# Kernel optimization log

Measured on AMD Instinct MI355X. Metric: run time of the kernel, lower is better.

Reference implementation:

```python
import jax, jax.numpy as jnp
import numpy as np

N, E, G = 5000, 10000, 200
EPS = 1e-5


def _nnconv(x, edge_attr, src, dst, w1, b1, w2, b2, root, bias, din, dout):
    # edge MLP -> per-edge weight matrix [E, din, dout]
    h = jax.nn.relu(edge_attr @ w1 + b1)
    We = (h @ w2 + b2).reshape(-1, din, dout)
    # gather source node feats, per-edge bmm, scatter-mean to targets
    msg = jnp.einsum('ei,eio->eo', x[src], We)  # [E, dout]
    s = jax.ops.segment_sum(msg, dst, num_segments=N)
    cnt = jax.ops.segment_sum(jnp.ones((msg.shape[0],), msg.dtype), dst, num_segments=N)
    agg = s / jnp.maximum(cnt, 1.0)[:, None]
    return agg + x @ root + bias


def _bn(x, g, b, m, v):
    return (x - m) * (g / jnp.sqrt(v + EPS)) + b


def setup_inputs() -> dict:
    key = jax.random.key(0)
    ks = iter(jax.random.split(key, 64))
    d = {}
    d['x'] = jax.random.normal(next(ks), (N, 15), jnp.float32)
    d['edge_attr'] = jax.random.normal(next(ks), (E, 3), jnp.float32)
    d['edge_index'] = jax.random.randint(next(ks), (2, E), 0, N, jnp.int32)
    d['batch'] = jnp.sort(jax.random.randint(next(ks), (N,), 0, G, jnp.int32))
    d['atom_num'] = jnp.zeros((G,), jnp.int32)
    dims = [(15, 64), (64, 128), (128, 256)]
    for l, (din, dout) in enumerate(dims, start=1):
        d[f'nn{l}_w1'] = jax.random.normal(next(ks), (3, 32), jnp.float32) * 0.1
        d[f'nn{l}_b1'] = jnp.zeros((32,), jnp.float32)
        d[f'nn{l}_w2'] = jax.random.normal(next(ks), (32, din * dout), jnp.float32) * 0.05
        d[f'nn{l}_b2'] = jnp.zeros((din * dout,), jnp.float32)
        d[f'root{l}'] = jax.random.normal(next(ks), (din, dout), jnp.float32) * 0.1
        d[f'bias{l}'] = jnp.zeros((dout,), jnp.float32)
        d[f'bn{l}_g'] = jnp.ones((dout,), jnp.float32)
        d[f'bn{l}_b'] = jnp.zeros((dout,), jnp.float32)
        d[f'bn{l}_m'] = jnp.zeros((dout,), jnp.float32)
        d[f'bn{l}_v'] = jnp.ones((dout,), jnp.float32)
    d['mlp_w'] = jax.random.normal(next(ks), (256, 200), jnp.float32) * 0.05
    d['mlp_b'] = jnp.zeros((200,), jnp.float32)
    return d


def reference(x, edge_attr, edge_index, batch, atom_num,
              nn1_w1, nn1_b1, nn1_w2, nn1_b2, root1, bias1, bn1_g, bn1_b, bn1_m, bn1_v,
              nn2_w1, nn2_b1, nn2_w2, nn2_b2, root2, bias2, bn2_g, bn2_b, bn2_m, bn2_v,
              nn3_w1, nn3_b1, nn3_w2, nn3_b2, root3, bias3, bn3_g, bn3_b, bn3_m, bn3_v,
              mlp_w, mlp_b):
    src, dst = edge_index[0], edge_index[1]
    h = _nnconv(x, edge_attr, src, dst, nn1_w1, nn1_b1, nn1_w2, nn1_b2, root1, bias1, 15, 64)
    h = jax.nn.relu(_bn(h, bn1_g, bn1_b, bn1_m, bn1_v))
    h = _nnconv(h, edge_attr, src, dst, nn2_w1, nn2_b1, nn2_w2, nn2_b2, root2, bias2, 64, 128)
    h = jax.nn.relu(_bn(h, bn2_g, bn2_b, bn2_m, bn2_v))
    h = _nnconv(h, edge_attr, src, dst, nn3_w1, nn3_b1, nn3_w2, nn3_b2, root3, bias3, 128, 256)
    h = jax.nn.relu(_bn(h, bn3_g, bn3_b, bn3_m, bn3_v))
    node_rep = h
    # per-graph node counts, exclusive cumulative offsets
    ones = jnp.ones((N,), h.dtype)
    counts = jax.ops.segment_sum(ones, batch, num_segments=G)  # [G]
    offsets = (jnp.cumsum(counts) - counts).astype(jnp.int32)
    idx = atom_num + offsets
    node_embedding = node_rep[idx]  # [G, 256]
    # global mean pool
    gsum = jax.ops.segment_sum(h, batch, num_segments=G)
    graph_embedding = gsum / jnp.maximum(counts, 1.0)[:, None]
    h_new = 0.5 * graph_embedding + node_embedding
    out = h_new @ mlp_w + mlp_b
    return out, node_embedding
```

## Files before the change

### kernel.cpp

```cpp
#include <hip/hip_runtime.h>
#include <stdint.h>

#define DEVINL __device__ __forceinline__

typedef __attribute__((ext_vector_type(8))) __bf16 bf16x8;
typedef __attribute__((ext_vector_type(8))) short s16x8;
typedef __attribute__((ext_vector_type(4))) float f32x4;

constexpr int NN = 5000;
constexpr int NE = 10000;
constexpr int NG = 200;
constexpr int BM = 64;
constexpr int MBLK = (NE + BM - 1) / BM;
constexpr int EROWS = MBLK * BM;
constexpr int SBLK = (NN + BM - 1) / BM;
constexpr int SROWS = SBLK * BM;
constexpr int NKP = 36;
constexpr int PHKT = 4;
constexpr int NBUF = 3;

DEVINL short f2bf(float f) {
  union { float f; unsigned u; } v; v.f = f;
  unsigned u = v.u + 0x7fffu + ((v.u >> 16) & 1u);
  return (short)(u >> 16);
}

DEVINL void gload16(const void* g, void* l) {
  __builtin_amdgcn_global_load_lds(
      (const __attribute__((address_space(1))) void*)g,
      (__attribute__((address_space(3))) void*)l, 16, 0, 0);
}


template <int DIN_DATA, int DIN_PAD, int DOUT>
DEVINL void buildB_one(int idx, const float* w2, const float* b2,
                       const float* root, short* Bp) {
  int cc = idx & 3;
  int n = (idx >> 2) % DOUT;
  int kt = (idx >> 2) / DOUT;
  int kap0 = kt * 32 + cc * 8;
  s16x8 v;
#pragma unroll
  for (int j = 0; j < 8; ++j) {
    int kap = kap0 + j;
    int k = kap / DIN_PAD, i = kap % DIN_PAD;
    float val = 0.f;
    if (i < DIN_DATA && k <= 33)
      val = (k < 32) ? w2[(size_t)(k * DIN_DATA + i) * DOUT + n]
                     : (k == 32) ? b2[(size_t)i * DOUT + n]
                                 : root[(size_t)i * DOUT + n];
    v[j] = f2bf(val);
  }
  int swz = cc ^ ((n >> 1) & 3);
  *(s16x8*)((char*)Bp + (size_t)kt * DOUT * 64 + n * 64 + swz * 16) = v;
}

constexpr int BCH1 = (NKP * 32 / 8) * 64;
constexpr int BCH2 = (NKP * 64 / 8) * 128;
constexpr int BCH3 = (NKP * 128 / 8) * 256;
constexpr int EMB = (EROWS + 255) / 256;
constexpr int PREPB = (NN * 32 + 255) / 256;
constexpr int BLDB = (BCH1 + BCH2 + BCH3 + 255) / 256;


__global__ void setup(const float* ea, const int* dst, const int* batch,
                      const float* x0,
                      const float* w1a, const float* b1a,
                      const float* w1b, const float* b1b,
                      const float* w1c, const float* b1c,
                      const float* w2a, const float* b2a, const float* ra,
                      const float* w2b, const float* b2b, const float* rb,
                      const float* w2c, const float* b2c, const float* rc,
                      short* hta, short* htb, short* htc,
                      short* Bp1, short* Bp2, short* Bp3,
                      float* cnt, float* gcnt, short* xbf0) {
  int b = blockIdx.x, t = threadIdx.x;
  if (b < 3 * EMB) {
    int L = b / EMB, eb = b % EMB;
    const float* w1 = (L == 0) ? w1a : (L == 1) ? w1b : w1c;
    const float* b1 = (L == 0) ? b1a : (L == 1) ? b1b : b1c;
    short* ht = (L == 0) ? hta : (L == 1) ? htb : htc;
    int e = eb * 256 + t;
    if (e >= EROWS) return;
    bool ve = e < NE;
    float a0 = 0, a1 = 0, a2 = 0;
    if (ve) { a0 = ea[e * 3]; a1 = ea[e * 3 + 1]; a2 = ea[e * 3 + 2]; }
    for (int k = 0; k < NKP; ++k) {
      float v = 0.f;
      if (ve) {
        if (k < 32) {
          float x = b1[k] + a0 * w1[k] + a1 * w1[32 + k] + a2 * w1[64 + k];
          v = x > 0.f ? x : 0.f;
        } else if (k == 32) {
          v = 1.0f;
        }
      }
      ht[(size_t)k * EROWS + e] = f2bf(v);
    }
  } else if (b < 3 * EMB + PREPB) {
    int idx = (b - 3 * EMB) * 256 + t;
    if (idx < NE) atomicAdd(&cnt[dst[idx]], 1.0f);
    if (idx < NN) atomicAdd(&gcnt[batch[idx]], 1.0f);
    if (idx < NN * 32) {
      int n = idx >> 5, i = idx & 31;
      xbf0[idx] = (i < 15) ? f2bf(x0[n * 15 + i]) : (short)0;
    }
  } else {
    int idx = (b - 3 * EMB - PREPB) * 256 + t;
    if (idx < BCH1) {
      buildB_one<15, 32, 64>(idx, w2a, b2a, ra, Bp1);
    } else if (idx < BCH1 + BCH2) {
      buildB_one<64, 64, 128>(idx - BCH1, w2b, b2b, rb, Bp2);
    } else if (idx < BCH1 + BCH2 + BCH3) {
      buildB_one<128, 128, 256>(idx - BCH1 - BCH2, w2c, b2c, rc, Bp3);
    }
  }
}


__global__ void node_scan(const float* cnt, int* noff, int* fill) {
  constexpr int PT = (NN + 1023) / 1024;
  __shared__ int s[1024];
  int t = threadIdx.x;
  int loc[PT];
  int sum = 0;
#pragma unroll
  for (int q = 0; q < PT; ++q) {
    int i = t * PT + q;
    loc[q] = sum;
    sum += (i < NN) ? (int)cnt[i] : 0;
  }
  s[t] = sum;
  __syncthreads();
  for (int d = 1; d < 1024; d <<= 1) {
    int u = (t >= d) ? s[t - d] : 0;
    __syncthreads();
    s[t] += u;
    __syncthreads();
  }
  int base = s[t] - sum;
#pragma unroll
  for (int q = 0; q < PT; ++q) {
    int i = t * PT + q;
    if (i < NN) { noff[i] = base + loc[q]; fill[i] = 0; }
  }
}

__global__ void csr_fill(const int* dst, const int* noff, int* fill, int* elist) {
  int e = blockIdx.x * 256 + threadIdx.x;
  if (e < NE) {
    int n = dst[e];
    int p = noff[n] + atomicAdd(&fill[n], 1);
    elist[p] = e;
  }
}


template <int DIN_PAD, int DOUT, int NSPLIT, int NKPE>
__launch_bounds__(512)
__global__ void fused_gemm(const short* xbf, const short* ht, const short* Bp,
                           const int* srcI, float* Pout) {
  constexpr int NI = DIN_PAD / 32;
  constexpr int ROWB = DIN_PAD * 2;
  constexpr int CHPR = ROWB / 16;
  constexpr int CHLOG = (CHPR == 4) ? 2 : (CHPR == 8) ? 3 : 4;
  constexpr int SWZM = (CHPR >= 8) ? 7 : 3;
  constexpr int DOUT_L = DOUT / NSPLIT;
  constexpr int MT = 2;
  constexpr int KT_TOTAL = NKPE * NI;
  constexpr int NPH = KT_TOTAL / PHKT;
  static_assert(KT_TOTAL % PHKT == 0, "phase align");
  static_assert(PHKT % NI == 0 || NI % PHKT == 0, "k align");
  constexpr int PHB = PHKT * DOUT_L * 64;
  constexpr int CPK = DOUT_L * 4;
  constexpr int CH = PHKT * CPK;
  constexpr int XGB = BM * ROWB;
  constexpr int SMB = (XGB > NBUF * PHB) ? XGB : NBUF * PHB;

  __shared__ __align__(16) char smem[SMB];
  __shared__ __align__(16) short hs[NKPE * BM];
  __shared__ int src_s[BM];

  const int t = threadIdx.x, lane = t & 63, w = t >> 6;
  const int wm = w >> 2, wn = w & 3;
  const bool isSelf = (blockIdx.x >= MBLK);
  const int m0 = (isSelf ? (blockIdx.x - MBLK) : blockIdx.x) * BM;
  const int bn0 = blockIdx.y * DOUT_L;
  if (t < BM) {
    int r = m0 + t;
    src_s[t] = isSelf ? ((r < NN) ? r : 0) : ((r < NE) ? srcI[r] : 0);
  }
  __syncthreads();

  constexpr int XCH = BM * CHPR;
#pragma unroll
  for (int rd = 0; rd < (XCH + 511) / 512; ++rd) {
    int L = rd * 512 + t;
    if (XCH % 512 == 0 || L < XCH) {
      int r = L >> CHLOG, pch = L & (CHPR - 1);
      int j = pch ^ (r & SWZM);
      gload16((const char*)xbf + (size_t)src_s[r] * ROWB + j * 16,
              (char*)smem + (size_t)L * 16);
    }
  }
  if (!isSelf && t < NKPE * (BM / 8)) {
    int kl = t >> 3, c = t & 7;
    gload16((const char*)ht + ((size_t)kl * EROWS + m0) * 2 + c * 16,
            (char*)hs + (size_t)t * 16);
  }
  __syncthreads();

  bf16x8 afr[NI][MT];
#pragma unroll
  for (int ii = 0; ii < NI; ++ii)
#pragma unroll
    for (int mt = 0; mt < MT; ++mt) {
      int r = wm * 32 + mt * 16 + (lane & 15);
      int c = ii * 4 + (lane >> 4);
      int pos = c ^ (r & SWZM);
      afr[ii][mt] = *(const bf16x8*)((const char*)smem + r * ROWB + pos * 16);
    }
  asm volatile("s_waitcnt lgkmcnt(0)" ::: "memory");
  __builtin_amdgcn_sched_barrier(0);
  __builtin_amdgcn_s_barrier();

  const char* Bg = (const char*)Bp + (size_t)bn0 * 64;

  f32x4 msg[MT], part[MT];
#pragma unroll
  for (int mt = 0; mt < MT; ++mt)
#pragma unroll
    for (int i = 0; i < 4; ++i) { msg[mt][i] = 0.f; part[mt][i] = 0.f; }

  if (isSelf) {
    constexpr int KT0 = 33 * NI;
    constexpr int CHS = NI * CPK;
#pragma unroll
    for (int cc = 0; cc < (CHS + 511) / 512; ++cc) {
      int idx = cc * 512 + t;
      if (CHS % 512 == 0 || idx < CHS) {
        int ktl = idx / CPK, win = idx % CPK;
        gload16(Bg + (size_t)(KT0 + ktl) * (DOUT * 64) + (size_t)win * 16,
                (char*)smem + (size_t)idx * 16);
      }
    }
    asm volatile("s_waitcnt vmcnt(0)" ::: "memory");
    __builtin_amdgcn_s_barrier();
    __builtin_amdgcn_sched_barrier(0);
#pragma unroll
    for (int j = 0; j < NI; ++j) {
      bf16x8 bfr;
      {
        int n = wn * 16 + (lane & 15);
        int cch = (lane >> 4) ^ ((n >> 1) & 3);
        bfr = *(const bf16x8*)((const char*)smem + j * (DOUT_L * 64) + n * 64 +
                               cch * 16);
      }
#pragma unroll
      for (int mt = 0; mt < MT; ++mt)
        msg[mt] = __builtin_amdgcn_mfma_f32_16x16x32_bf16(afr[j][mt], bfr,
                                                          msg[mt], 0, 0, 0);
    }
    float* P = Pout + (size_t)(EROWS + m0) * DOUT + bn0;
#pragma unroll
    for (int mt = 0; mt < MT; ++mt) {
      int col = wn * 16 + (lane & 15);
#pragma unroll
      for (int reg = 0; reg < 4; ++reg) {
        int r = wm * 32 + mt * 16 + (lane >> 4) * 4 + reg;
        P[(size_t)r * DOUT + col] = msg[mt][reg];
      }
    }
    return;
  }

  auto stageB = [&](int ph, int buf) {
    char* dstB = (char*)smem + buf * PHB;
#pragma unroll
    for (int cc = 0; cc < CH / 512; ++cc) {
      int idx = cc * 512 + t;
      int ktl = idx / CPK;
      int win = idx % CPK;
      gload16(Bg + (size_t)(ph * PHKT + ktl) * (DOUT * 64) + (size_t)win * 16,
              dstB + (size_t)idx * 16);
    }
  };

  stageB(0, 0);
  if (NPH > 1) stageB(1, 1);
  if (NPH > 2) stageB(2, 2);
  for (int ph = 0; ph < NPH; ++ph) {
    if (ph + 2 < NPH) {
      asm volatile("s_waitcnt vmcnt(4)" ::: "memory");
    } else if (ph + 1 < NPH) {
      asm volatile("s_waitcnt vmcnt(2)" ::: "memory");
    } else {
      asm volatile("s_waitcnt vmcnt(0)" ::: "memory");
    }
    __builtin_amdgcn_s_barrier();
    __builtin_amdgcn_sched_barrier(0);
    const char* buf = (const char*)smem + (ph % NBUF) * PHB;
#pragma unroll
    for (int j = 0; j < PHKT; ++j) {
      const int kt = ph * PHKT + j;
      bf16x8 bfr;
      {
        int n = wn * 16 + (lane & 15);
        int cch = (lane >> 4) ^ ((n >> 1) & 3);
        bfr = *(const bf16x8*)(buf + j * (DOUT_L * 64) + n * 64 + cch * 16);
      }
#pragma unroll
      for (int mt = 0; mt < MT; ++mt)
        part[mt] = __builtin_amdgcn_mfma_f32_16x16x32_bf16(
            afr[j % NI][mt], bfr, part[mt], 0, 0, 0);
      if ((j % NI) == NI - 1) {
        int kl = kt / NI;
#pragma unroll
        for (int mt = 0; mt < MT; ++mt) {
          int rb = wm * 32 + mt * 16 + (lane >> 4) * 4;
          ushort4 hv = *(const ushort4*)((const char*)hs + (size_t)(kl * BM + rb) * 2);
          float h0, h1, h2, h3;
          { union { unsigned u; float f; } c;
            c.u = (unsigned)hv.x << 16; h0 = c.f;
            c.u = (unsigned)hv.y << 16; h1 = c.f;
            c.u = (unsigned)hv.z << 16; h2 = c.f;
            c.u = (unsigned)hv.w << 16; h3 = c.f; }
          msg[mt][0] += h0 * part[mt][0];
          msg[mt][1] += h1 * part[mt][1];
          msg[mt][2] += h2 * part[mt][2];
          msg[mt][3] += h3 * part[mt][3];
#pragma unroll
          for (int i = 0; i < 4; ++i) part[mt][i] = 0.f;
        }
      }
    }
    __builtin_amdgcn_sched_barrier(0);
    __builtin_amdgcn_s_barrier();
    if (ph + NBUF < NPH) stageB(ph + NBUF, (ph + NBUF) % NBUF);
  }
  float* P = Pout + (size_t)m0 * DOUT + bn0;
#pragma unroll
  for (int mt = 0; mt < MT; ++mt) {
    int col = wn * 16 + (lane & 15);
#pragma unroll
    for (int reg = 0; reg < 4; ++reg) {
      int r = wm * 32 + mt * 16 + (lane >> 4) * 4 + reg;
      P[(size_t)r * DOUT + col] = msg[mt][reg];
    }
  }
}


template <int DOUT>
__launch_bounds__(256)
__global__ void post_node(const float* P, const float* cnt, const int* noff,
                          const int* elist, const float* bias, const float* bg,
                          const float* bb, const float* bm, const float* bv,
                          float* xout, short* xbf) {
  constexpr int NPB = 8;
  constexpr int OS = 256 / DOUT;
  constexpr int NPT = NPB / OS;
  __shared__ int offs[NPB], cnts[NPB];
  int n0 = blockIdx.x * NPB;
  int t = threadIdx.x;
  int o = t % DOUT;
  int ng = t / DOUT;
  if (t < NPB) {
    int n = n0 + t;
    offs[t] = (n < NN) ? noff[n] : 0;
    cnts[t] = (n < NN) ? (int)cnt[n] : 0;
  }
  __syncthreads();
  float bi = bias[o];
  float scale = bg[o] * rsqrtf(bv[o] + 1e-5f);
  float mo = bm[o], bo = bb[o];
#pragma unroll
  for (int q = 0; q < NPT; ++q) {
    int nn = ng + q * OS;
    int n = n0 + nn;
    if (n >= NN) continue;
    int off = offs[nn], c = cnts[nn];
    float s = 0.f;
    for (int j = 0; j < c; ++j) {
      int e = elist[off + j];
      s += P[(size_t)e * DOUT + o];
    }
    float selfv = P[(size_t)(EROWS + n) * DOUT + o];
    float accv = s / fmaxf((float)c, 1.f) + selfv + bi;
    float v = (accv - mo) * scale + bo;
    v = v > 0.f ? v : 0.f;
    if (xout) xout[(size_t)n * DOUT + o] = v;
    if (xbf) xbf[(size_t)n * DOUT + o] = f2bf(v);
  }
}


__global__ void finish(const float* gcnt, const int* atom, const float* x3,
                       const float* mw, const float* mb, float* out) {
  __shared__ float red[256];
  __shared__ float hnew[256];
  int g = blockIdx.x, t = threadIdx.x;
  red[t] = (t < NG && t < g) ? gcnt[t] : 0.f;
  __syncthreads();
#pragma unroll
  for (int d = 128; d > 0; d >>= 1) {
    if (t < d) red[t] += red[t + d];
    __syncthreads();
  }
  int st = (int)red[0];
  int cn = (int)gcnt[g];
  int id = st + atom[g];
  id = id < 0 ? 0 : (id > NN - 1 ? NN - 1 : id);
  float s = 0.f;
  for (int n = st; n < st + cn; ++n) s += x3[(size_t)n * 256 + t];
  float ge = s / fmaxf((float)cn, 1.f);
  float ne = x3[(size_t)id * 256 + t];
  out[40000 + g * 256 + t] = ne;
  hnew[t] = 0.5f * ge + ne;
  __syncthreads();
  if (t < 200) {
    float a = mb[t];
#pragma unroll 8
    for (int oo = 0; oo < 256; ++oo) a += hnew[oo] * mw[(size_t)oo * 200 + t];
    out[g * 200 + t] = a;
  }
}


template <int DIN_PAD, int DOUT, int NSPLIT, int NKPE>
static void run_layer(void* const* d_in, int l, const int* srcI,
                      const short* xbf_in, float* xout_f32, short* xbf_out,
                      float* Pbuf, const float* cnt, const int* noff,
                      const int* elist, const short* ht, const short* Bp,
                      hipStream_t stream) {
  int base = 5 + (l - 1) * 10;
  const float* bias = (const float*)d_in[base + 5];
  const float* bg = (const float*)d_in[base + 6];
  const float* bb = (const float*)d_in[base + 7];
  const float* bm = (const float*)d_in[base + 8];
  const float* bv = (const float*)d_in[base + 9];

  fused_gemm<DIN_PAD, DOUT, NSPLIT, NKPE>
      <<<dim3(MBLK + SBLK, NSPLIT), 512, 0, stream>>>(xbf_in, ht, Bp, srcI, Pbuf);
  post_node<DOUT><<<(NN + 7) / 8, 256, 0, stream>>>(
      Pbuf, cnt, noff, elist, bias, bg, bb, bm, bv, xout_f32, xbf_out);
}

extern "C" void kernel_launch(void* const* d_in, const int* in_sizes, int n_in,
                              void* d_out, int out_size, void* d_ws, size_t ws_size,
                              hipStream_t stream) {
  (void)in_sizes; (void)n_in; (void)out_size; (void)ws_size;
  const float* x0 = (const float*)d_in[0];
  const float* ea = (const float*)d_in[1];
  const int* eidx = (const int*)d_in[2];
  const int* batch = (const int*)d_in[3];
  const int* atom = (const int*)d_in[4];
  const float* mw = (const float*)d_in[35];
  const float* mb = (const float*)d_in[36];
  const int* srcI = eidx;
  const int* dstI = eidx + NE;
  float* out = (float*)d_out;

  char* p = (char*)d_ws;
  auto alloc = [&](size_t bytes) {
    char* r = p;
    p += (bytes + 255) & ~size_t(255);
    return r;
  };
  float* xA = (float*)alloc((size_t)NN * 256 * 4);
  float* Pbuf = (float*)alloc((size_t)(EROWS + SROWS) * 256 * 4);
  float* cnt = (float*)alloc(NN * 4);
  int* noff = (int*)alloc(NN * 4);
  int* fill = (int*)alloc(NN * 4);
  int* elist = (int*)alloc(NE * 4);
  float* gcnt = (float*)alloc(NG * 4);
  short* ht1 = (short*)alloc((size_t)NKP * EROWS * 2);
  short* ht2 = (short*)alloc((size_t)NKP * EROWS * 2);
  short* ht3 = (short*)alloc((size_t)NKP * EROWS * 2);
  short* Bp1 = (short*)alloc((size_t)NKP * 32 * 64 * 2);
  short* Bp2 = (short*)alloc((size_t)NKP * 64 * 128 * 2);
  short* Bp3 = (short*)alloc((size_t)NKP * 128 * 256 * 2);
  short* xbf0 = (short*)alloc((size_t)NN * 32 * 2);
  short* xbfA = (short*)alloc((size_t)NN * 64 * 2);
  short* xbfB = (short*)alloc((size_t)NN * 128 * 2);

  hipMemsetAsync(cnt, 0, NN * 4, stream);
  hipMemsetAsync(gcnt, 0, NG * 4, stream);
  setup<<<3 * EMB + PREPB + BLDB, 256, 0, stream>>>(
      ea, dstI, batch, x0,
      (const float*)d_in[5], (const float*)d_in[6],
      (const float*)d_in[15], (const float*)d_in[16],
      (const float*)d_in[25], (const float*)d_in[26],
      (const float*)d_in[7], (const float*)d_in[8], (const float*)d_in[9],
      (const float*)d_in[17], (const float*)d_in[18], (const float*)d_in[19],
      (const float*)d_in[27], (const float*)d_in[28], (const float*)d_in[29],
      ht1, ht2, ht3, Bp1, Bp2, Bp3, cnt, gcnt, xbf0);
  node_scan<<<1, 1024, 0, stream>>>(cnt, noff, fill);
  csr_fill<<<(NE + 255) / 256, 256, 0, stream>>>(dstI, noff, fill, elist);

  run_layer<32, 64, 1, 36>(d_in, 1, srcI, xbf0, (float*)nullptr, xbfA, Pbuf,
                           cnt, noff, elist, ht1, Bp1, stream);
  run_layer<64, 128, 2, 34>(d_in, 2, srcI, xbfA, (float*)nullptr, xbfB, Pbuf,
                            cnt, noff, elist, ht2, Bp2, stream);
  run_layer<128, 256, 4, 33>(d_in, 3, srcI, xbfB, xA, (short*)nullptr, Pbuf,
                             cnt, noff, elist, ht3, Bp3, stream);

  finish<<<NG, 256, 0, stream>>>(gcnt, atom, xA, mw, mb, out);
}
```

Baseline: 260.9 us.

## Fold CSR build into setup, use fp32 edge hidden, larger layer-3 tile

Moves the node count, prefix scan, CSR fill and graph-count work into one extra block of the setup kernel using shared-memory atomics. This removes two memsets and the separate node_scan and csr_fill launches. The edge-MLP hidden values are now stored in fp32 instead of bf16, which drops the unpack step in the GEMM at the cost of twice the hidden-value traffic and LDS. The GEMM takes its row tile as a template parameter and layer 3 uses 128-row tiles. post_node now derives counts from consecutive offsets and stages the edge list in shared memory when it fits.

New measurement: 258.7 us. Within noise of the previous version (-0.8%).

```diff
diff --git a/kernel.cpp b/kernel.cpp
--- a/kernel.cpp
+++ b/kernel.cpp
@@ -10,11 +10,8 @@
 constexpr int NN = 5000;
 constexpr int NE = 10000;
 constexpr int NG = 200;
-constexpr int BM = 64;
-constexpr int MBLK = (NE + BM - 1) / BM;
-constexpr int EROWS = MBLK * BM;
-constexpr int SBLK = (NN + BM - 1) / BM;
-constexpr int SROWS = SBLK * BM;
+constexpr int EROWS = 10112;
+constexpr int SROWSMX = 5120;
 constexpr int NKP = 36;
 constexpr int PHKT = 4;
 constexpr int NBUF = 3;
@@ -58,29 +55,29 @@
 constexpr int BCH1 = (NKP * 32 / 8) * 64;
 constexpr int BCH2 = (NKP * 64 / 8) * 128;
 constexpr int BCH3 = (NKP * 128 / 8) * 256;
-constexpr int EMB = (EROWS + 255) / 256;
-constexpr int PREPB = (NN * 32 + 255) / 256;
-constexpr int BLDB = (BCH1 + BCH2 + BCH3 + 255) / 256;
-
-
-__global__ void setup(const float* ea, const int* dst, const int* batch,
-                      const float* x0,
-                      const float* w1a, const float* b1a,
-                      const float* w1b, const float* b1b,
-                      const float* w1c, const float* b1c,
-                      const float* w2a, const float* b2a, const float* ra,
-                      const float* w2b, const float* b2b, const float* rb,
-                      const float* w2c, const float* b2c, const float* rc,
-                      short* hta, short* htb, short* htc,
-                      short* Bp1, short* Bp2, short* Bp3,
-                      float* cnt, float* gcnt, short* xbf0) {
+constexpr int EMB = (EROWS + 1023) / 1024;
+constexpr int CASTB = (NN * 32 + 1023) / 1024;
+constexpr int BLDB = (BCH1 + BCH2 + BCH3 + 1023) / 1024;
+constexpr int SETUPB = 3 * EMB + CASTB + BLDB + 1;
+
+
+__global__ __launch_bounds__(1024) void setup(
+    const float* ea, const int* dst, const int* batch, const float* x0,
+    const float* w1a, const float* b1a, const float* w1b, const float* b1b,
+    const float* w1c, const float* b1c,
+    const float* w2a, const float* b2a, const float* ra,
+    const float* w2b, const float* b2b, const float* rb,
+    const float* w2c, const float* b2c, const float* rc,
+    float* hta, float* htb, float* htc,
+    short* Bp1, short* Bp2, short* Bp3,
+    short* xbf0, int* noff, int* elist, float* gcnt) {
   int b = blockIdx.x, t = threadIdx.x;
   if (b < 3 * EMB) {
     int L = b / EMB, eb = b % EMB;
     const float* w1 = (L == 0) ? w1a : (L == 1) ? w1b : w1c;
     const float* b1 = (L == 0) ? b1a : (L == 1) ? b1b : b1c;
-    short* ht = (L == 0) ? hta : (L == 1) ? htb : htc;
-    int e = eb * 256 + t;
+    float* ht = (L == 0) ? hta : (L == 1) ? htb : htc;
+    int e = eb * 1024 + t;
     if (e >= EROWS) return;
     bool ve = e < NE;
     float a0 = 0, a1 = 0, a2 = 0;
@@ -95,18 +92,16 @@
           v = 1.0f;
         }
       }
-      ht[(size_t)k * EROWS + e] = f2bf(v);
-    }
-  } else if (b < 3 * EMB + PREPB) {
-    int idx = (b - 3 * EMB) * 256 + t;
-    if (idx < NE) atomicAdd(&cnt[dst[idx]], 1.0f);
-    if (idx < NN) atomicAdd(&gcnt[batch[idx]], 1.0f);
+      ht[(size_t)k * EROWS + e] = v;
+    }
+  } else if (b < 3 * EMB + CASTB) {
+    int idx = (b - 3 * EMB) * 1024 + t;
     if (idx < NN * 32) {
       int n = idx >> 5, i = idx & 31;
       xbf0[idx] = (i < 15) ? f2bf(x0[n * 15 + i]) : (short)0;
     }
-  } else {
-    int idx = (b - 3 * EMB - PREPB) * 256 + t;
+  } else if (b < 3 * EMB + CASTB + BLDB) {
+    int idx = (b - 3 * EMB - CASTB) * 1024 + t;
     if (idx < BCH1) {
       buildB_one<15, 32, 64>(idx, w2a, b2a, ra, Bp1);
     } else if (idx < BCH1 + BCH2) {
@@ -114,59 +109,68 @@
     } else if (idx < BCH1 + BCH2 + BCH3) {
       buildB_one<128, 128, 256>(idx - BCH1 - BCH2, w2c, b2c, rc, Bp3);
     }
-  }
-}
-
-
-__global__ void node_scan(const float* cnt, int* noff, int* fill) {
-  constexpr int PT = (NN + 1023) / 1024;
-  __shared__ int s[1024];
-  int t = threadIdx.x;
-  int loc[PT];
-  int sum = 0;
-#pragma unroll
-  for (int q = 0; q < PT; ++q) {
-    int i = t * PT + q;
-    loc[q] = sum;
-    sum += (i < NN) ? (int)cnt[i] : 0;
-  }
-  s[t] = sum;
-  __syncthreads();
-  for (int d = 1; d < 1024; d <<= 1) {
-    int u = (t >= d) ? s[t - d] : 0;
+  } else {
+    __shared__ int cntL[NN];
+    __shared__ int sS[1024];
+    __shared__ int gcntL[NG];
+    for (int i = t; i < NN; i += 1024) cntL[i] = 0;
+    if (t < NG) gcntL[t] = 0;
     __syncthreads();
-    s[t] += u;
+    for (int e = t; e < NE; e += 1024) atomicAdd(&cntL[dst[e]], 1);
+    for (int i = t; i < NN; i += 1024) atomicAdd(&gcntL[batch[i]], 1);
     __syncthreads();
-  }
-  int base = s[t] - sum;
-#pragma unroll
-  for (int q = 0; q < PT; ++q) {
-    int i = t * PT + q;
-    if (i < NN) { noff[i] = base + loc[q]; fill[i] = 0; }
-  }
-}
-
-__global__ void csr_fill(const int* dst, const int* noff, int* fill, int* elist) {
-  int e = blockIdx.x * 256 + threadIdx.x;
-  if (e < NE) {
-    int n = dst[e];
-    int p = noff[n] + atomicAdd(&fill[n], 1);
-    elist[p] = e;
-  }
-}
-
-
-template <int DIN_PAD, int DOUT, int NSPLIT, int NKPE>
+    constexpr int PT = (NN + 1023) / 1024;
+    int loc[PT];
+    int sum = 0;
+#pragma unroll
+    for (int q = 0; q < PT; ++q) {
+      int i = t * PT + q;
+      loc[q] = sum;
+      sum += (i < NN) ? cntL[i] : 0;
+    }
+    sS[t] = sum;
+    __syncthreads();
+    for (int d = 1; d < 1024; d <<= 1) {
+      int u = (t >= d) ? sS[t - d] : 0;
+      __syncthreads();
+      sS[t] += u;
+      __syncthreads();
+    }
+    int base = sS[t] - sum;
+#pragma unroll
+    for (int q = 0; q < PT; ++q) {
+      int i = t * PT + q;
+      if (i < NN) {
+        int v = base + loc[q];
+        noff[i] = v;
+        cntL[i] = v;
+      }
+    }
+    if (t < 16) noff[NN + t] = NE;
+    if (t < NG) gcnt[t] = (float)gcntL[t];
+    __syncthreads();
+    for (int e = t; e < NE; e += 1024) {
+      int n = dst[e];
+      int p = atomicAdd(&cntL[n], 1);
+      elist[p] = e;
+    }
+  }
+}
+
+
+template <int BMT, int DIN_PAD, int DOUT, int NSPLIT, int NKPE>
 __launch_bounds__(512)
-__global__ void fused_gemm(const short* xbf, const short* ht, const short* Bp,
+__global__ void fused_gemm(const short* xbf, const float* ht, const short* Bp,
                            const int* srcI, float* Pout) {
+  constexpr int MBLK = (NE + BMT - 1) / BMT;
   constexpr int NI = DIN_PAD / 32;
   constexpr int ROWB = DIN_PAD * 2;
   constexpr int CHPR = ROWB / 16;
   constexpr int CHLOG = (CHPR == 4) ? 2 : (CHPR == 8) ? 3 : 4;
   constexpr int SWZM = (CHPR >= 8) ? 7 : 3;
   constexpr int DOUT_L = DOUT / NSPLIT;
-  constexpr int MT = 2;
+  constexpr int MT = BMT / 32;
+  constexpr int WROWS = MT * 16;
   constexpr int KT_TOTAL = NKPE * NI;
   constexpr int NPH = KT_TOTAL / PHKT;
   static_assert(KT_TOTAL % PHKT == 0, "phase align");
@@ -174,25 +178,25 @@
   constexpr int PHB = PHKT * DOUT_L * 64;
   constexpr int CPK = DOUT_L * 4;
   constexpr int CH = PHKT * CPK;
-  constexpr int XGB = BM * ROWB;
+  constexpr int XGB = BMT * ROWB;
   constexpr int SMB = (XGB > NBUF * PHB) ? XGB : NBUF * PHB;
 
   __shared__ __align__(16) char smem[SMB];
-  __shared__ __align__(16) short hs[NKPE * BM];
-  __shared__ int src_s[BM];
+  __shared__ __align__(16) float hs[NKPE * BMT];
+  __shared__ int src_s[BMT];
 
   const int t = threadIdx.x, lane = t & 63, w = t >> 6;
   const int wm = w >> 2, wn = w & 3;
   const bool isSelf = (blockIdx.x >= MBLK);
-  const int m0 = (isSelf ? (blockIdx.x - MBLK) : blockIdx.x) * BM;
+  const int m0 = (isSelf ? (blockIdx.x - MBLK) : blockIdx.x) * BMT;
   const int bn0 = blockIdx.y * DOUT_L;
-  if (t < BM) {
+  if (t < BMT) {
     int r = m0 + t;
     src_s[t] = isSelf ? ((r < NN) ? r : 0) : ((r < NE) ? srcI[r] : 0);
   }
   __syncthreads();
 
-  constexpr int XCH = BM * CHPR;
+  constexpr int XCH = BMT * CHPR;
 #pragma unroll
   for (int rd = 0; rd < (XCH + 511) / 512; ++rd) {
     int L = rd * 512 + t;
@@ -203,10 +207,13 @@
               (char*)smem + (size_t)L * 16);
     }
   }
-  if (!isSelf && t < NKPE * (BM / 8)) {
-    int kl = t >> 3, c = t & 7;
-    gload16((const char*)ht + ((size_t)kl * EROWS + m0) * 2 + c * 16,
-            (char*)hs + (size_t)t * 16);
+  if (!isSelf) {
+    constexpr int CHH = NKPE * BMT / 4;
+    for (int idx = t; idx < CHH; idx += 512) {
+      int kl = idx / (BMT / 4), c = idx % (BMT / 4);
+      gload16((const char*)ht + ((size_t)kl * EROWS + m0 + c * 4) * 4,
+              (char*)hs + (size_t)idx * 16);
+    }
   }
   __syncthreads();
 
@@ -215,7 +222,7 @@
   for (int ii = 0; ii < NI; ++ii)
 #pragma unroll
     for (int mt = 0; mt < MT; ++mt) {
-      int r = wm * 32 + mt * 16 + (lane & 15);
+      int r = wm * WROWS + mt * 16 + (lane & 15);
       int c = ii * 4 + (lane >> 4);
       int pos = c ^ (r & SWZM);
       afr[ii][mt] = *(const bf16x8*)((const char*)smem + r * ROWB + pos * 16);
@@ -267,7 +274,7 @@
       int col = wn * 16 + (lane & 15);
 #pragma unroll
       for (int reg = 0; reg < 4; ++reg) {
-        int r = wm * 32 + mt * 16 + (lane >> 4) * 4 + reg;
+        int r = wm * WROWS + mt * 16 + (lane >> 4) * 4 + reg;
         P[(size_t)r * DOUT + col] = msg[mt][reg];
       }
     }
@@ -317,18 +324,12 @@
         int kl = kt / NI;
 #pragma unroll
         for (int mt = 0; mt < MT; ++mt) {
-          int rb = wm * 32 + mt * 16 + (lane >> 4) * 4;
-          ushort4 hv = *(const ushort4*)((const char*)hs + (size_t)(kl * BM + rb) * 2);
-          float h0, h1, h2, h3;
-          { union { unsigned u; float f; } c;
-            c.u = (unsigned)hv.x << 16; h0 = c.f;
-            c.u = (unsigned)hv.y << 16; h1 = c.f;
-            c.u = (unsigned)hv.z << 16; h2 = c.f;
-            c.u = (unsigned)hv.w << 16; h3 = c.f; }
-          msg[mt][0] += h0 * part[mt][0];
-          msg[mt][1] += h1 * part[mt][1];
-          msg[mt][2] += h2 * part[mt][2];
-          msg[mt][3] += h3 * part[mt][3];
+          int rb = wm * WROWS + mt * 16 + (lane >> 4) * 4;
+          float4 hv = *(const float4*)(hs + (size_t)kl * BMT + rb);
+          msg[mt][0] += hv.x * part[mt][0];
+          msg[mt][1] += hv.y * part[mt][1];
+          msg[mt][2] += hv.z * part[mt][2];
+          msg[mt][3] += hv.w * part[mt][3];
 #pragma unroll
           for (int i = 0; i < 4; ++i) part[mt][i] = 0.f;
         }
@@ -344,7 +345,7 @@
     int col = wn * 16 + (lane & 15);
 #pragma unroll
     for (int reg = 0; reg < 4; ++reg) {
-      int r = wm * 32 + mt * 16 + (lane >> 4) * 4 + reg;
+      int r = wm * WROWS + mt * 16 + (lane >> 4) * 4 + reg;
       P[(size_t)r * DOUT + col] = msg[mt][reg];
     }
   }
@@ -353,24 +354,27 @@
 
 template <int DOUT>
 __launch_bounds__(256)
-__global__ void post_node(const float* P, const float* cnt, const int* noff,
-                          const int* elist, const float* bias, const float* bg,
-                          const float* bb, const float* bm, const float* bv,
-                          float* xout, short* xbf) {
+__global__ void post_node(const float* P, const int* noff, const int* elist,
+                          const float* bias, const float* bg, const float* bb,
+                          const float* bm, const float* bv, float* xout,
+                          short* xbf) {
   constexpr int NPB = 8;
   constexpr int OS = 256 / DOUT;
   constexpr int NPT = NPB / OS;
-  __shared__ int offs[NPB], cnts[NPB];
+  __shared__ int offs[NPB + 1];
+  __shared__ int es[256];
   int n0 = blockIdx.x * NPB;
   int t = threadIdx.x;
-  int o = t % DOUT;
-  int ng = t / DOUT;
-  if (t < NPB) {
-    int n = n0 + t;
-    offs[t] = (n < NN) ? noff[n] : 0;
-    cnts[t] = (n < NN) ? (int)cnt[n] : 0;
-  }
+  if (t <= NPB) offs[t] = noff[n0 + t];
   __syncthreads();
+  int base = offs[0];
+  int range = offs[NPB] - base;
+  bool fit = (range <= 256);
+  if (fit) {
+    for (int i = t; i < range; i += 256) es[i] = elist[base + i];
+  }
+  __syncthreads();
+  int o = t % DOUT, ng = t / DOUT;
   float bi = bias[o];
   float scale = bg[o] * rsqrtf(bv[o] + 1e-5f);
   float mo = bm[o], bo = bb[o];
@@ -379,10 +383,10 @@
     int nn = ng + q * OS;
     int n = n0 + nn;
     if (n >= NN) continue;
-    int off = offs[nn], c = cnts[nn];
+    int off0 = offs[nn], c = offs[nn + 1] - off0;
     float s = 0.f;
     for (int j = 0; j < c; ++j) {
-      int e = elist[off + j];
+      int e = fit ? es[off0 - base + j] : elist[off0 + j];
       s += P[(size_t)e * DOUT + o];
     }
     float selfv = P[(size_t)(EROWS + n) * DOUT + o];
@@ -427,12 +431,11 @@
 }
 
 
-template <int DIN_PAD, int DOUT, int NSPLIT, int NKPE>
+template <int BMT, int DIN_PAD, int DOUT, int NSPLIT, int NKPE>
 static void run_layer(void* const* d_in, int l, const int* srcI,
                       const short* xbf_in, float* xout_f32, short* xbf_out,
-                      float* Pbuf, const float* cnt, const int* noff,
-                      const int* elist, const short* ht, const short* Bp,
-                      hipStream_t stream) {
+                      float* Pbuf, const int* noff, const int* elist,
+                      const float* ht, const short* Bp, hipStream_t stream) {
   int base = 5 + (l - 1) * 10;
   const float* bias = (const float*)d_in[base + 5];
   const float* bg = (const float*)d_in[base + 6];
@@ -440,10 +443,12 @@
   const float* bm = (const float*)d_in[base + 8];
   const float* bv = (const float*)d_in[base + 9];
 
-  fused_gemm<DIN_PAD, DOUT, NSPLIT, NKPE>
+  constexpr int MBLK = (NE + BMT - 1) / BMT;
+  constexpr int SBLK = (NN + BMT - 1) / BMT;
+  fused_gemm<BMT, DIN_PAD, DOUT, NSPLIT, NKPE>
       <<<dim3(MBLK + SBLK, NSPLIT), 512, 0, stream>>>(xbf_in, ht, Bp, srcI, Pbuf);
   post_node<DOUT><<<(NN + 7) / 8, 256, 0, stream>>>(
-      Pbuf, cnt, noff, elist, bias, bg, bb, bm, bv, xout_f32, xbf_out);
+      Pbuf, noff, elist, bias, bg, bb, bm, bv, xout_f32, xbf_out);
 }
 
 extern "C" void kernel_launch(void* const* d_in, const int* in_sizes, int n_in,
@@ -468,15 +473,13 @@
     return r;
   };
   float* xA = (float*)alloc((size_t)NN * 256 * 4);
-  float* Pbuf = (float*)alloc((size_t)(EROWS + SROWS) * 256 * 4);
-  float* cnt = (float*)alloc(NN * 4);
-  int* noff = (int*)alloc(NN * 4);
-  int* fill = (int*)alloc(NN * 4);
+  float* Pbuf = (float*)alloc((size_t)(EROWS + SROWSMX) * 256 * 4);
+  int* noff = (int*)alloc((NN + 16) * 4);
   int* elist = (int*)alloc(NE * 4);
   float* gcnt = (float*)alloc(NG * 4);
-  short* ht1 = (short*)alloc((size_t)NKP * EROWS * 2);
-  short* ht2 = (short*)alloc((size_t)NKP * EROWS * 2);
-  short* ht3 = (short*)alloc((size_t)NKP * EROWS * 2);
+  float* ht1 = (float*)alloc((size_t)NKP * EROWS * 4);
+  float* ht2 = (float*)alloc((size_t)NKP * EROWS * 4);
+  float* ht3 = (float*)alloc((size_t)NKP * EROWS * 4);
   short* Bp1 = (short*)alloc((size_t)NKP * 32 * 64 * 2);
   short* Bp2 = (short*)alloc((size_t)NKP * 64 * 128 * 2);
   short* Bp3 = (short*)alloc((size_t)NKP * 128 * 256 * 2);
@@ -484,9 +487,7 @@
   short* xbfA = (short*)alloc((size_t)NN * 64 * 2);
   short* xbfB = (short*)alloc((size_t)NN * 128 * 2);
 
-  hipMemsetAsync(cnt, 0, NN * 4, stream);
-  hipMemsetAsync(gcnt, 0, NG * 4, stream);
-  setup<<<3 * EMB + PREPB + BLDB, 256, 0, stream>>>(
+  setup<<<SETUPB, 1024, 0, stream>>>(
       ea, dstI, batch, x0,
       (const float*)d_in[5], (const float*)d_in[6],
       (const float*)d_in[15], (const float*)d_in[16],
@@ -494,16 +495,14 @@
       (const float*)d_in[7], (const float*)d_in[8], (const float*)d_in[9],
       (const float*)d_in[17], (const float*)d_in[18], (const float*)d_in[19],
       (const float*)d_in[27], (const float*)d_in[28], (const float*)d_in[29],
-      ht1, ht2, ht3, Bp1, Bp2, Bp3, cnt, gcnt, xbf0);
-  node_scan<<<1, 1024, 0, stream>>>(cnt, noff, fill);
-  csr_fill<<<(NE + 255) / 256, 256, 0, stream>>>(dstI, noff, fill, elist);
-
-  run_layer<32, 64, 1, 36>(d_in, 1, srcI, xbf0, (float*)nullptr, xbfA, Pbuf,
-                           cnt, noff, elist, ht1, Bp1, stream);
-  run_layer<64, 128, 2, 34>(d_in, 2, srcI, xbfA, (float*)nullptr, xbfB, Pbuf,
-                            cnt, noff, elist, ht2, Bp2, stream);
-  run_layer<128, 256, 4, 33>(d_in, 3, srcI, xbfB, xA, (short*)nullptr, Pbuf,
-                             cnt, noff, elist, ht3, Bp3, stream);
+      ht1, ht2, ht3, Bp1, Bp2, Bp3, xbf0, noff, elist, gcnt);
+
+  run_layer<64, 32, 64, 1, 36>(d_in, 1, srcI, xbf0, (float*)nullptr, xbfA, Pbuf,
+                               noff, elist, ht1, Bp1, stream);
+  run_layer<64, 64, 128, 2, 34>(d_in, 2, srcI, xbfA, (float*)nullptr, xbfB, Pbuf,
+                                noff, elist, ht2, Bp2, stream);
+  run_layer<128, 128, 256, 4, 33>(d_in, 3, srcI, xbfB, xA, (short*)nullptr, Pbuf,
+                                  noff, elist, ht3, Bp3, stream);
 
   finish<<<NG, 256, 0, stream>>>(gcnt, atom, xA, mw, mb, out);
 }
```
